# Optimization experiments

Hardware: AMD Instinct MI355X
Metric: run time of the kernel (lower is better)

Reference implementation:

```python
import jax, jax.numpy as jnp
import numpy as np

HID, H, P = 1024, 16, 50  # hid_dim, n_heads, max_relative_position
DH = HID // H


def _rel_idx(len_q, len_k):
    # [Lq, Lk] clipped relative-distance indices into the (2P+1)-row table
    d = jnp.arange(len_k)[None, :] - jnp.arange(len_q)[:, None]
    return jnp.clip(d, -P, P) + P


def setup_inputs() -> dict:
    key = jax.random.key(0)
    ks = jax.random.split(key, 13)
    L, B = 2048, 2
    s = 0.02
    return {
        "query": jax.random.normal(ks[0], (L, B, HID), jnp.float32),
        "key": jax.random.normal(ks[1], (L, B, HID), jnp.float32),
        "value": jax.random.normal(ks[2], (L, B, HID), jnp.float32),
        "Wq": jax.random.normal(ks[3], (HID, HID), jnp.float32) * s,
        "bq": jax.random.normal(ks[4], (HID,), jnp.float32) * s,
        "Wk": jax.random.normal(ks[5], (HID, HID), jnp.float32) * s,
        "bk": jax.random.normal(ks[6], (HID,), jnp.float32) * s,
        "Wv": jax.random.normal(ks[7], (HID, HID), jnp.float32) * s,
        "bv": jax.random.normal(ks[8], (HID,), jnp.float32) * s,
        "Wo": jax.random.normal(ks[9], (HID, HID), jnp.float32) * s,
        "bo": jax.random.normal(ks[10], (HID,), jnp.float32) * s,
        "rel_k": jax.random.normal(ks[11], (2 * P + 1, DH), jnp.float32) * s,
        "rel_v": jax.random.normal(ks[12], (2 * P + 1, DH), jnp.float32) * s,
    }


def reference(query, key, value, Wq, bq, Wk, bk, Wv, bv, Wo, bo, rel_k, rel_v):
    # inputs are seq-first [L, B, hid]; torch code transposes to batch-first
    q = jnp.swapaxes(query, 0, 1)  # [B, Lq, hid]
    k = jnp.swapaxes(key, 0, 1)
    v = jnp.swapaxes(value, 0, 1)
    B, Lq, _ = q.shape
    Lk = k.shape[1]

    q = q @ Wq.T + bq
    k = k @ Wk.T + bk
    v = v @ Wv.T + bv

    # split heads: [B, H, L, DH]
    qh = q.reshape(B, Lq, H, DH).transpose(0, 2, 1, 3)
    kh = k.reshape(B, Lk, H, DH).transpose(0, 2, 1, 3)
    vh = v.reshape(B, Lk, H, DH).transpose(0, 2, 1, 3)

    idx = _rel_idx(Lq, Lk)
    Rk = rel_k[idx]  # [Lq, Lk, DH]
    Rv = rel_v[idx]  # [Lq, Lk, DH]

    attn1 = jnp.einsum('bhqd,bhkd->bhqk', qh, kh)
    attn2 = jnp.einsum('bhqd,qkd->bhqk', qh, Rk)
    scale = jnp.asarray(np.sqrt(DH), qh.dtype)
    attn = jax.nn.softmax((attn1 + attn2) / scale, axis=-1)  # dropout p=0 -> identity

    w1 = jnp.einsum('bhqk,bhkd->bhqd', attn, vh)
    w2 = jnp.einsum('bhqk,qkd->bhqd', attn, Rv)
    x = (w1 + w2).transpose(0, 2, 1, 3).reshape(B, Lq, HID)
    x = x @ Wo.T + bo
    return jnp.swapaxes(x, 0, 1)  # [Lq, B, hid]
```

## Files before the change

kernel.cpp:

```cpp
#include <hip/hip_runtime.h>


#define LSEQ 2048
#define HIDDIM 1024
#define NH 16
#define DHD 64
#define NREL 101
#define PMAX 50
#define SCL 0.18033688011112042f

typedef __attribute__((ext_vector_type(8))) __bf16 bf16x8;
typedef __attribute__((ext_vector_type(4))) float f32x4;

#define MFMA(A, B, C) __builtin_amdgcn_mfma_f32_16x16x32_bf16(A, B, C, 0, 0, 0)

__device__ __forceinline__ unsigned short f2bf(float f) {
  unsigned int u = __builtin_bit_cast(unsigned int, f);
  u += 0x7fffu + ((u >> 16) & 1u);
  return (unsigned short)(u >> 16);
}
__device__ __forceinline__ float bflo(unsigned int u) { return __builtin_bit_cast(float, u << 16); }

__device__ __forceinline__ uint4 pack8(float4 f0, float4 f1) {
  uint4 o;
  o.x = (unsigned)f2bf(f0.x) | ((unsigned)f2bf(f0.y) << 16);
  o.y = (unsigned)f2bf(f0.z) | ((unsigned)f2bf(f0.w) << 16);
  o.z = (unsigned)f2bf(f1.x) | ((unsigned)f2bf(f1.y) << 16);
  o.w = (unsigned)f2bf(f1.z) | ((unsigned)f2bf(f1.w) << 16);
  return o;
}

__device__ __forceinline__ void gload16(const unsigned short* g, unsigned short* l) {
  __builtin_amdgcn_global_load_lds(
      (const __attribute__((address_space(1))) unsigned int*)g,
      (__attribute__((address_space(3))) unsigned int*)l, 16, 0, 0);
}

__global__ void cast_w4(const float* __restrict__ s0, const float* __restrict__ s1,
                        const float* __restrict__ s2, const float* __restrict__ s3,
                        unsigned short* __restrict__ dst) {
  const int e = (blockIdx.x * 256 + threadIdx.x) * 8;
  const int g = e >> 20;
  const float* s = (g == 0) ? s0 : (g == 1) ? s1 : (g == 2) ? s2 : s3;
  const int o = e & 0xFFFFF;
  const float4 f0 = *(const float4*)(s + o);
  const float4 f1 = *(const float4*)(s + o + 4);
  *(uint4*)(dst + e) = pack8(f0, f1);
}

__global__ void cast_x3(const float* __restrict__ q, const float* __restrict__ k,
                        const float* __restrict__ v,
                        unsigned short* __restrict__ dq, unsigned short* __restrict__ dk,
                        unsigned short* __restrict__ dv) {
  const int gid = blockIdx.x * 256 + threadIdx.x;
  const int segi = gid >> 19;
  const int e = (gid & 0x7FFFF) * 8;
  const float* s = (segi == 0) ? q : (segi == 1) ? k : v;
  unsigned short* dst = (segi == 0) ? dq : (segi == 1) ? dk : dv;
  const int m = e >> 10, kk = e & 1023;
  const int b = m >> 11, l = m & 2047;
  const float* sp = s + (size_t)((l << 1) + b) * HIDDIM + kk;
  const float4 f0 = *(const float4*)sp;
  const float4 f1 = *(const float4*)(sp + 4);
  *(uint4*)(dst + e) = pack8(f0, f1);
}

__global__ void cast_rk_kernel(const float* __restrict__ src, unsigned short* __restrict__ dst) {
  const int e = blockIdx.x * 256 + threadIdx.x;
  if (e >= 112 * 64) return;
  dst[e] = (e < NREL * 64) ? f2bf(src[e]) : (unsigned short)0;
}

__global__ void cast_rv_kernel(const float* __restrict__ src, unsigned short* __restrict__ dst) {
  const int e = blockIdx.x * 256 + threadIdx.x;
  if (e >= 64 * 128) return;
  const int d = e >> 7, j = e & 127;
  dst[e] = (j < NREL) ? f2bf(src[j * DHD + d]) : (unsigned short)0;
}

__global__ __launch_bounds__(256, 3) void gemm_qkv(
    const unsigned short* __restrict__ Xq, const unsigned short* __restrict__ Xk,
    const unsigned short* __restrict__ Xv, const unsigned short* __restrict__ Wcat,
    const float* __restrict__ bq, const float* __restrict__ bk, const float* __restrict__ bv,
    unsigned short* __restrict__ Qb, unsigned short* __restrict__ Kb,
    unsigned short* __restrict__ Vgt) {
  __shared__ __align__(16) unsigned short SH[17408];
  unsigned short* LA = SH;
  unsigned short* LB = SH + 8192;

  const int tid = threadIdx.x;
  const int seg = blockIdx.x >> 8;
  const int t = blockIdx.x & 255;
  const int m0 = (t >> 3) * 128, n0 = (t & 7) * 128;

  const unsigned short* A = (seg == 0) ? Xq : (seg == 1) ? Xk : Xv;
  const unsigned short* W = Wcat + ((size_t)seg << 20);
  const float* bias = (seg == 0) ? bq : (seg == 1) ? bk : bv;

  const int lane = tid & 63, w = tid >> 6;
  const int c = lane & 15, quad = lane >> 4;

  const int srow = w * 32 + (lane >> 3);
  const int scol = ((lane & 7) ^ (lane >> 3)) << 3;
  const unsigned short* pA = A + (size_t)(m0 + srow) * 1024 + scol;
  const unsigned short* pW = W + (size_t)(n0 + srow) * 1024 + scol;
  unsigned short* lA = LA + w * 2048;
  unsigned short* lB = LB + w * 2048;

  const int wr = w >> 1, wc = w & 1;
  const int cx = (c & 7) << 3;

  f32x4 acc[4][4] = {};

  for (int k0 = 0; k0 < 1024; k0 += 64) {
#pragma unroll
    for (int i = 0; i < 4; i++) {
      gload16(pA + k0 + i * 8192, lA + i * 512);
      gload16(pW + k0 + i * 8192, lB + i * 512);
    }
    __syncthreads();
#pragma unroll
    for (int ks = 0; ks < 2; ks++) {
      bf16x8 af[4], bfr[4];
#pragma unroll
      for (int f = 0; f < 4; f++) {
        af[f]  = *(const bf16x8*)&LA[(wr * 64 + f * 16 + c) * 64 + ((ks * 32 + quad * 8) ^ cx)];
        bfr[f] = *(const bf16x8*)&LB[(wc * 64 + f * 16 + c) * 64 + ((ks * 32 + quad * 8) ^ cx)];
      }
#pragma unroll
      for (int i = 0; i < 4; i++)
#pragma unroll
        for (int j = 0; j < 4; j++)
          acc[i][j] = MFMA(af[i], bfr[j], acc[i][j]);
    }
    __syncthreads();
  }

  const int b = m0 >> 11, l0 = m0 & 2047;
  const int h0 = n0 >> 6;
  if (seg < 2) {
    unsigned short* out = seg ? Kb : Qb;
#pragma unroll
    for (int i = 0; i < 4; i++)
#pragma unroll
      for (int j = 0; j < 4; j++) {
        const int nl = wc * 64 + j * 16 + c;
        const float bv_ = bias[n0 + nl];
        const int h = h0 + (nl >> 6), d = nl & 63;
#pragma unroll
        for (int r = 0; r < 4; r++) {
          const int l = l0 + wr * 64 + i * 16 + quad * 4 + r;
          out[((size_t)((b * NH + h) * LSEQ + l) << 6) + d] = f2bf(acc[i][j][r] + bv_);
        }
      }
  } else {
    unsigned short* Ct = SH;
#pragma unroll
    for (int i = 0; i < 4; i++)
#pragma unroll
      for (int j = 0; j < 4; j++) {
        const int nl = wc * 64 + j * 16 + c;
        const float bv_ = bias[n0 + nl];
#pragma unroll
        for (int r = 0; r < 4; r++) {
          const int ml = wr * 64 + i * 16 + quad * 4 + r;
          Ct[nl * 136 + ml] = f2bf(acc[i][j][r] + bv_);
        }
      }
    __syncthreads();
    const int dr = tid >> 1, lc = (tid & 1) * 64;
    const int h = h0 + (dr >> 6), dd = dr & 63;
    unsigned short* dst = Vgt + ((size_t)((b * NH + h) * 64 + dd)) * LSEQ + l0 + lc;
    const unsigned short* src = Ct + dr * 136 + lc;
#pragma unroll
    for (int u = 0; u < 8; u++)
      *(uint4*)(dst + u * 8) = *(const uint4*)(src + u * 8);
  }
}

template <int MODE>
__global__ __launch_bounds__(256, 4) void gemm64(
    const unsigned short* __restrict__ A,
    const unsigned short* __restrict__ W,
    const float* __restrict__ bias,
    float* __restrict__ outF,
    unsigned short* __restrict__ outB) {
  constexpr int K = 1024;
  __shared__ unsigned short As[64 * 72];
  __shared__ unsigned short Bs[64 * 72];
  const int tid = threadIdx.x;
  const int tm = blockIdx.x >> 4, tn = blockIdx.x & 15;
  const int m0 = tm * 64, n0 = tn * 64;
  const int lane = tid & 63, wave = tid >> 6;
  const int wm = (wave >> 1) * 32, wn = (wave & 1) * 32;
  const int qr = lane & 15, quad = lane >> 4;
  const int sr = tid >> 3, sc = (tid & 7) * 8;
  f32x4 acc[2][2] = {};
  for (int k0 = 0; k0 < K; k0 += 64) {
    *(uint4*)&As[sr * 72 + sc]        = *(const uint4*)&A[(size_t)(m0 + sr) * K + k0 + sc];
    *(uint4*)&As[(sr + 32) * 72 + sc] = *(const uint4*)&A[(size_t)(m0 + sr + 32) * K + k0 + sc];
    *(uint4*)&Bs[sr * 72 + sc]        = *(const uint4*)&W[(size_t)(n0 + sr) * K + k0 + sc];
    *(uint4*)&Bs[(sr + 32) * 72 + sc] = *(const uint4*)&W[(size_t)(n0 + sr + 32) * K + k0 + sc];
    __syncthreads();
#pragma unroll
    for (int ks = 0; ks < 64; ks += 32) {
      bf16x8 a0 = *(const bf16x8*)&As[(wm + qr) * 72 + ks + quad * 8];
      bf16x8 a1 = *(const bf16x8*)&As[(wm + 16 + qr) * 72 + ks + quad * 8];
      bf16x8 b0 = *(const bf16x8*)&Bs[(wn + qr) * 72 + ks + quad * 8];
      bf16x8 b1 = *(const bf16x8*)&Bs[(wn + 16 + qr) * 72 + ks + quad * 8];
      acc[0][0] = MFMA(a0, b0, acc[0][0]);
      acc[0][1] = MFMA(a0, b1, acc[0][1]);
      acc[1][0] = MFMA(a1, b0, acc[1][0]);
      acc[1][1] = MFMA(a1, b1, acc[1][1]);
    }
    __syncthreads();
  }
#pragma unroll
  for (int i = 0; i < 2; i++)
#pragma unroll
    for (int j = 0; j < 2; j++) {
      const int n = n0 + wn + 16 * j + qr;
      const float bv = bias[n];
#pragma unroll
      for (int rr = 0; rr < 4; rr++) {
        const int m = m0 + wm + 16 * i + quad * 4 + rr;
        const float v = acc[i][j][rr] + bv;
        const int b = m >> 11, l = m & 2047;
        if (MODE == 1) {
          outF[(size_t)((l << 1) + b) * HIDDIM + n] = v;
        }
      }
    }
}

#define KT 32
__global__ __launch_bounds__(256, 4) void attn_mfma(
    const unsigned short* __restrict__ Qb,
    const unsigned short* __restrict__ Kb,
    const unsigned short* __restrict__ Vgt,
    const unsigned short* __restrict__ RKb,
    const unsigned short* __restrict__ RVb,
    unsigned short* __restrict__ outB) {
  __shared__ __align__(16) unsigned short SH[20416];
  unsigned short* Kst = SH;
  unsigned short* Tb  = SH + 7424;
  unsigned short* SrS = SH + 13952;

  const int tid = threadIdx.x;
  const int xcd = blockIdx.x & 7, slot = blockIdx.x >> 3;
  const int bh = (slot >> 5) * 8 + xcd;
  const int q0 = (slot & 31) * 64;

  const int lane = tid & 63, wq = tid >> 6;
  const int c = lane & 15, quad = lane >> 4;
  const size_t base = (size_t)bh * (LSEQ * DHD);
  const unsigned short* Qp = Qb + base;
  const unsigned short* Kp = Kb + base;
  const unsigned short* Vp = Vgt + base;
  unsigned short* Ptw = SH + 4608 + wq * 704;

  const int qrow_w = q0 + wq * 16;
  const int srow = quad * 4;
  const int wrow0 = wq * 16 + srow;

  {
    unsigned* tz = (unsigned*)(Tb + wq * 1632);
    for (int e = lane; e < 816; e += 64) tz[e] = 0u;
  }

  const bf16x8 aq0 = *(const bf16x8*)&Qp[(size_t)(qrow_w + c) * DHD + quad * 8];
  const bf16x8 aq1 = *(const bf16x8*)&Qp[(size_t)(qrow_w + c) * DHD + 32 + quad * 8];

#pragma unroll
  for (int jt = 0; jt < 7; jt++) {
    bf16x8 b0 = *(const bf16x8*)&RKb[(jt * 16 + c) * DHD + quad * 8];
    bf16x8 b1 = *(const bf16x8*)&RKb[(jt * 16 + c) * DHD + 32 + quad * 8];
    f32x4 s4 = {};
    s4 = MFMA(aq0, b0, s4);
    s4 = MFMA(aq1, b1, s4);
    const int jc = jt * 16 + c;
    if (jc < NREL) {
#pragma unroll
      for (int r = 0; r < 4; r++) SrS[(wrow0 + r) * NREL + jc] = f2bf(s4[r]);
    }
  }

  float Srlo[4], Srhi[4];
#pragma unroll
  for (int r = 0; r < 4; r++) {
    Srlo[r] = bflo((unsigned)SrS[(wrow0 + r) * NREL + 0]);
    Srhi[r] = bflo((unsigned)SrS[(wrow0 + r) * NREL + 100]);
  }

  float rsum[4] = {0.f, 0.f, 0.f, 0.f};
  float lows[4] = {0.f, 0.f, 0.f, 0.f}, highs[4] = {0.f, 0.f, 0.f, 0.f};
  f32x4 Od[4] = {};

  const int strow = tid >> 3, stcol = (tid & 7) * 8;

  {
    uint4 k0r = *(const uint4*)&Kp[(size_t)strow * DHD + stcol];
    *(uint4*)&Kst[strow * 72 + stcol] = k0r;
  }
  __syncthreads();

  for (int it = 0; it < 64; ++it) {
    const int k0 = it * KT;
    const int cur = (it & 1) * 2304;
    uint4 kreg;
    if (it < 63) kreg = *(const uint4*)&Kp[(size_t)(k0 + KT + strow) * DHD + stcol];
    bf16x8 vf[4];
#pragma unroll
    for (int t = 0; t < 4; t++)
      vf[t] = *(const bf16x8*)&Vp[(size_t)(t * 16 + c) * LSEQ + k0 + quad * 8];

    const bf16x8 bk00 = *(const bf16x8*)&Kst[cur + c * 72 + quad * 8];
    const bf16x8 bk01 = *(const bf16x8*)&Kst[cur + c * 72 + 32 + quad * 8];
    const bf16x8 bk10 = *(const bf16x8*)&Kst[cur + (16 + c) * 72 + quad * 8];
    const bf16x8 bk11 = *(const bf16x8*)&Kst[cur + (16 + c) * 72 + 32 + quad * 8];
    f32x4 s0 = {}, s1 = {};
    s0 = MFMA(aq0, bk00, s0);
    s0 = MFMA(aq1, bk01, s0);
    s1 = MFMA(aq0, bk10, s1);
    s1 = MFMA(aq1, bk11, s1);

    const int mode = (k0 + KT - 1 <= qrow_w - 50) ? 0 : (k0 >= qrow_w + 65) ? 2 : 1;

#pragma unroll
    for (int kt = 0; kt < 2; kt++) {
      const f32x4 s = kt ? s1 : s0;
      const int kcol = k0 + kt * 16 + c;
#pragma unroll
      for (int r = 0; r < 4; r++) {
        float srv;
        int j = -1;
        if (mode == 0) srv = Srlo[r];
        else if (mode == 2) srv = Srhi[r];
        else {
          int dl = kcol - (qrow_w + srow + r);
          dl = dl < -PMAX ? -PMAX : (dl > PMAX ? PMAX : dl);
          j = dl + PMAX;
          srv = bflo((unsigned)SrS[(wrow0 + r) * NREL + j]);
        }
        const float p = exp2f((s[r] + srv) * SCL);
        const unsigned short pb = f2bf(p);
        const float pf = bflo((unsigned)pb);
        rsum[r] += pf;
        if (mode == 0) lows[r] += pf;
        else if (mode == 2) highs[r] += pf;
        else {
          if (j == 0) lows[r] += pf;
          else if (j == 100) highs[r] += pf;
          else Tb[(wrow0 + r) * 102 + j] = pb;
        }
        Ptw[(srow + r) * 44 + kt * 16 + c] = pb;
      }
    }

    const uint2 aplo = *(const uint2*)&Ptw[c * 44 + quad * 8];
    const uint2 aphi = *(const uint2*)&Ptw[c * 44 + quad * 8 + 4];
    const bf16x8 ap = __builtin_bit_cast(bf16x8, (uint4){aplo.x, aplo.y, aphi.x, aphi.y});
#pragma unroll
    for (int t = 0; t < 4; t++)
      Od[t] = MFMA(ap, vf[t], Od[t]);

    if (it < 63) *(uint4*)&Kst[(cur ^ 2304) + strow * 72 + stcol] = kreg;
    __syncthreads();
  }

#pragma unroll
  for (int m = 1; m < 16; m <<= 1) {
#pragma unroll
    for (int r = 0; r < 4; r++) {
      rsum[r] += __shfl_xor(rsum[r], m, 64);
      lows[r] += __shfl_xor(lows[r], m, 64);
      highs[r] += __shfl_xor(highs[r], m, 64);
    }
  }
  if (c == 0) {
#pragma unroll
    for (int r = 0; r < 4; r++) {
      Tb[(wrow0 + r) * 102 + 0]   = f2bf(lows[r]);
      Tb[(wrow0 + r) * 102 + 100] = f2bf(highs[r]);
    }
  }
  __syncthreads();

#pragma unroll
  for (int kc = 0; kc < 4; kc++) {
    unsigned short a8[8];
#pragma unroll
    for (int jj = 0; jj < 8; jj++) {
      const int j = kc * 32 + quad * 8 + jj;
      a8[jj] = (j <= 100) ? Tb[(wq * 16 + c) * 102 + j] : (unsigned short)0;
    }
    bf16x8 at;
#pragma unroll
    for (int jj = 0; jj < 8; jj++) at[jj] = __builtin_bit_cast(__bf16, a8[jj]);
#pragma unroll
    for (int t = 0; t < 4; t++) {
      const bf16x8 bv = *(const bf16x8*)&RVb[(t * 16 + c) * 128 + kc * 32 + quad * 8];
      Od[t] = MFMA(at, bv, Od[t]);
    }
  }

  const int b = bh >> 4, h = bh & 15;
#pragma unroll
  for (int r = 0; r < 4; r++) {
    const float inv = 1.f / rsum[r];
    const int qg = q0 + wq * 16 + srow + r;
    unsigned short* op = outB + (size_t)(b * LSEQ + qg) * HIDDIM + h * DHD + c;
#pragma unroll
    for (int t = 0; t < 4; t++) op[t * 16] = f2bf(Od[t][r] * inv);
  }
}

extern "C" void kernel_launch(void* const* d_in, const int* in_sizes, int n_in,
                              void* d_out, int out_size, void* d_ws, size_t ws_size,
                              hipStream_t stream) {
  const float* query = (const float*)d_in[0];
  const float* key   = (const float*)d_in[1];
  const float* value = (const float*)d_in[2];
  const float* Wq = (const float*)d_in[3];  const float* bq = (const float*)d_in[4];
  const float* Wk = (const float*)d_in[5];  const float* bk = (const float*)d_in[6];
  const float* Wv = (const float*)d_in[7];  const float* bv = (const float*)d_in[8];
  const float* Wo = (const float*)d_in[9];  const float* bo = (const float*)d_in[10];
  const float* relk = (const float*)d_in[11];
  const float* relv = (const float*)d_in[12];
  float* out = (float*)d_out;

  char* w = (char*)d_ws;
  const size_t MB = 1ull << 20;
  unsigned short* Wcat = (unsigned short*)(w + 0 * MB);
  unsigned short* Wob  = (unsigned short*)(w + 6 * MB);
  unsigned short* Xq   = (unsigned short*)(w + 8 * MB);
  unsigned short* Qb   = (unsigned short*)(w + 16 * MB);
  unsigned short* Kb   = (unsigned short*)(w + 24 * MB);
  unsigned short* Vgt  = (unsigned short*)(w + 32 * MB);
  unsigned short* AOb  = Xq;
  unsigned short* RKb  = Wcat;
  unsigned short* RVb  = (unsigned short*)(w + 2 * MB);
  unsigned short* Xk = (unsigned short*)out;
  unsigned short* Xv = (unsigned short*)out + (4u << 20);

  cast_w4<<<2048, 256, 0, stream>>>(Wq, Wk, Wv, Wo, Wcat);
  cast_x3<<<6144, 256, 0, stream>>>(query, key, value, Xq, Xk, Xv);
  gemm_qkv<<<768, 256, 0, stream>>>(Xq, Xk, Xv, Wcat, bq, bk, bv, Qb, Kb, Vgt);
  cast_rk_kernel<<<28, 256, 0, stream>>>(relk, RKb);
  cast_rv_kernel<<<32, 256, 0, stream>>>(relv, RVb);
  attn_mfma<<<1024, 256, 0, stream>>>(Qb, Kb, Vgt, RKb, RVb, AOb);
  gemm64<1><<<1024, 256, 0, stream>>>(AOb, Wob, bo, out, nullptr);
}
```

Before: 334.8 us.

## Transpose score MFMA so each lane owns a query row, use packed bf16 converts

Swaps the MFMA operand order in the QK and Q·relK products so the score tile is transposed and each lane holds one query row. The softmax row sums then reduce with fewer shuffles, and the relative-bias and Tb tables become per-wave buffers. The change also uses the v_cvt_pk_bf16_f32 instruction for packing and writes P as packed uint2 stores. Block-wide __syncthreads before the rel-V stage are replaced by an LDS waitcnt fence. The aim is to cut scalar bf16 conversion, LDS traffic and shuffle work in the inner softmax loop, at the cost of more intricate per-lane indexing and reliance on per-wave LDS visibility.

```diff
diff --git a/kernel.cpp b/kernel.cpp
--- a/kernel.cpp
+++ b/kernel.cpp
@@ -13,6 +13,7 @@
 typedef __attribute__((ext_vector_type(4))) float f32x4;
 
 #define MFMA(A, B, C) __builtin_amdgcn_mfma_f32_16x16x32_bf16(A, B, C, 0, 0, 0)
+#define LDS_FENCE() asm volatile("s_waitcnt lgkmcnt(0)" ::: "memory")
 
 __device__ __forceinline__ unsigned short f2bf(float f) {
   unsigned int u = __builtin_bit_cast(unsigned int, f);
@@ -20,6 +21,14 @@
   return (unsigned short)(u >> 16);
 }
 __device__ __forceinline__ float bflo(unsigned int u) { return __builtin_bit_cast(float, u << 16); }
+
+__device__ __forceinline__ unsigned cvtpk(float lo, float hi) {
+  unsigned r;
+  asm("v_cvt_pk_bf16_f32 %0, %1, %2" : "=v"(r) : "v"(lo), "v"(hi));
+  return r;
+}
+__device__ __forceinline__ float pklo(unsigned pk) { return __builtin_bit_cast(float, pk << 16); }
+__device__ __forceinline__ float pkhi(unsigned pk) { return __builtin_bit_cast(float, pk & 0xffff0000u); }
 
 __device__ __forceinline__ uint4 pack8(float4 f0, float4 f1) {
   uint4 o;
@@ -241,10 +250,8 @@
     const unsigned short* __restrict__ RKb,
     const unsigned short* __restrict__ RVb,
     unsigned short* __restrict__ outB) {
-  __shared__ __align__(16) unsigned short SH[20416];
+  __shared__ __align__(16) unsigned short SH[20480];
   unsigned short* Kst = SH;
-  unsigned short* Tb  = SH + 7424;
-  unsigned short* SrS = SH + 13952;
 
   const int tid = threadIdx.x;
   const int xcd = blockIdx.x & 7, slot = blockIdx.x >> 3;
@@ -253,19 +260,21 @@
 
   const int lane = tid & 63, wq = tid >> 6;
   const int c = lane & 15, quad = lane >> 4;
+  unsigned short* Ptw = SH + 4608 + wq * 640;
+  unsigned short* Tb  = SH + 7168 + wq * 1664;
+  unsigned short* SrS = SH + 13824 + wq * 1664;
+
   const size_t base = (size_t)bh * (LSEQ * DHD);
   const unsigned short* Qp = Qb + base;
   const unsigned short* Kp = Kb + base;
   const unsigned short* Vp = Vgt + base;
-  unsigned short* Ptw = SH + 4608 + wq * 704;
 
   const int qrow_w = q0 + wq * 16;
-  const int srow = quad * 4;
-  const int wrow0 = wq * 16 + srow;
 
   {
-    unsigned* tz = (unsigned*)(Tb + wq * 1632);
-    for (int e = lane; e < 816; e += 64) tz[e] = 0u;
+    uint4 z = {0u, 0u, 0u, 0u};
+    uint4* tz = (uint4*)(SH + 7168);
+    for (int e = tid; e < 832; e += 256) tz[e] = z;
   }
 
   const bf16x8 aq0 = *(const bf16x8*)&Qp[(size_t)(qrow_w + c) * DHD + quad * 8];
@@ -273,36 +282,30 @@
 
 #pragma unroll
   for (int jt = 0; jt < 7; jt++) {
-    bf16x8 b0 = *(const bf16x8*)&RKb[(jt * 16 + c) * DHD + quad * 8];
-    bf16x8 b1 = *(const bf16x8*)&RKb[(jt * 16 + c) * DHD + 32 + quad * 8];
+    const bf16x8 rk0 = *(const bf16x8*)&RKb[(jt * 16 + c) * DHD + quad * 8];
+    const bf16x8 rk1 = *(const bf16x8*)&RKb[(jt * 16 + c) * DHD + 32 + quad * 8];
     f32x4 s4 = {};
-    s4 = MFMA(aq0, b0, s4);
-    s4 = MFMA(aq1, b1, s4);
-    const int jc = jt * 16 + c;
-    if (jc < NREL) {
-#pragma unroll
-      for (int r = 0; r < 4; r++) SrS[(wrow0 + r) * NREL + jc] = f2bf(s4[r]);
-    }
-  }
-
-  float Srlo[4], Srhi[4];
-#pragma unroll
-  for (int r = 0; r < 4; r++) {
-    Srlo[r] = bflo((unsigned)SrS[(wrow0 + r) * NREL + 0]);
-    Srhi[r] = bflo((unsigned)SrS[(wrow0 + r) * NREL + 100]);
-  }
-
-  float rsum[4] = {0.f, 0.f, 0.f, 0.f};
-  float lows[4] = {0.f, 0.f, 0.f, 0.f}, highs[4] = {0.f, 0.f, 0.f, 0.f};
-  f32x4 Od[4] = {};
+    s4 = MFMA(rk0, aq0, s4);
+    s4 = MFMA(rk1, aq1, s4);
+    const int jb = jt * 16 + quad * 4;
+    const unsigned p01 = cvtpk(s4[0], s4[1]);
+    const unsigned p23 = cvtpk(s4[2], s4[3]);
+    if (jb <= 102)     *(unsigned*)&SrS[c * 104 + jb] = p01;
+    if (jb + 2 <= 102) *(unsigned*)&SrS[c * 104 + jb + 2] = p23;
+  }
 
   const int strow = tid >> 3, stcol = (tid & 7) * 8;
-
   {
     uint4 k0r = *(const uint4*)&Kp[(size_t)strow * DHD + stcol];
     *(uint4*)&Kst[strow * 72 + stcol] = k0r;
   }
   __syncthreads();
+
+  const float srvlo = bflo((unsigned)SrS[c * 104 + 0]);
+  const float srvhi = bflo((unsigned)SrS[c * 104 + 100]);
+
+  float lows = 0.f, highs = 0.f, mids = 0.f;
+  f32x4 Od[4] = {};
 
   for (int it = 0; it < 64; ++it) {
     const int k0 = it * KT;
@@ -314,52 +317,70 @@
     for (int t = 0; t < 4; t++)
       vf[t] = *(const bf16x8*)&Vp[(size_t)(t * 16 + c) * LSEQ + k0 + quad * 8];
 
-    const bf16x8 bk00 = *(const bf16x8*)&Kst[cur + c * 72 + quad * 8];
-    const bf16x8 bk01 = *(const bf16x8*)&Kst[cur + c * 72 + 32 + quad * 8];
-    const bf16x8 bk10 = *(const bf16x8*)&Kst[cur + (16 + c) * 72 + quad * 8];
-    const bf16x8 bk11 = *(const bf16x8*)&Kst[cur + (16 + c) * 72 + 32 + quad * 8];
+    const bf16x8 ka00 = *(const bf16x8*)&Kst[cur + c * 72 + quad * 8];
+    const bf16x8 ka01 = *(const bf16x8*)&Kst[cur + c * 72 + 32 + quad * 8];
+    const bf16x8 ka10 = *(const bf16x8*)&Kst[cur + (16 + c) * 72 + quad * 8];
+    const bf16x8 ka11 = *(const bf16x8*)&Kst[cur + (16 + c) * 72 + 32 + quad * 8];
     f32x4 s0 = {}, s1 = {};
-    s0 = MFMA(aq0, bk00, s0);
-    s0 = MFMA(aq1, bk01, s0);
-    s1 = MFMA(aq0, bk10, s1);
-    s1 = MFMA(aq1, bk11, s1);
+    s0 = MFMA(ka00, aq0, s0);
+    s0 = MFMA(ka01, aq1, s0);
+    s1 = MFMA(ka10, aq0, s1);
+    s1 = MFMA(ka11, aq1, s1);
 
     const int mode = (k0 + KT - 1 <= qrow_w - 50) ? 0 : (k0 >= qrow_w + 65) ? 2 : 1;
 
-#pragma unroll
-    for (int kt = 0; kt < 2; kt++) {
-      const f32x4 s = kt ? s1 : s0;
-      const int kcol = k0 + kt * 16 + c;
+    unsigned pkA0, pkA1, pkB0, pkB1;
+    if (mode != 1) {
+      const float srv = (mode == 0) ? srvlo : srvhi;
+      const float e0 = exp2f((s0[0] + srv) * SCL);
+      const float e1 = exp2f((s0[1] + srv) * SCL);
+      const float e2 = exp2f((s0[2] + srv) * SCL);
+      const float e3 = exp2f((s0[3] + srv) * SCL);
+      const float e4 = exp2f((s1[0] + srv) * SCL);
+      const float e5 = exp2f((s1[1] + srv) * SCL);
+      const float e6 = exp2f((s1[2] + srv) * SCL);
+      const float e7 = exp2f((s1[3] + srv) * SCL);
+      pkA0 = cvtpk(e0, e1); pkA1 = cvtpk(e2, e3);
+      pkB0 = cvtpk(e4, e5); pkB1 = cvtpk(e6, e7);
+      const float sq = ((pklo(pkA0) + pkhi(pkA0)) + (pklo(pkA1) + pkhi(pkA1)))
+                     + ((pklo(pkB0) + pkhi(pkB0)) + (pklo(pkB1) + pkhi(pkB1)));
+      if (mode == 0) lows += sq; else highs += sq;
+    } else {
+      const int kb0 = k0 + quad * 4 - (qrow_w + c) + 50;
+      float ee[8]; int jj[8];
 #pragma unroll
       for (int r = 0; r < 4; r++) {
-        float srv;
-        int j = -1;
-        if (mode == 0) srv = Srlo[r];
-        else if (mode == 2) srv = Srhi[r];
-        else {
-          int dl = kcol - (qrow_w + srow + r);
-          dl = dl < -PMAX ? -PMAX : (dl > PMAX ? PMAX : dl);
-          j = dl + PMAX;
-          srv = bflo((unsigned)SrS[(wrow0 + r) * NREL + j]);
-        }
-        const float p = exp2f((s[r] + srv) * SCL);
-        const unsigned short pb = f2bf(p);
-        const float pf = bflo((unsigned)pb);
-        rsum[r] += pf;
-        if (mode == 0) lows[r] += pf;
-        else if (mode == 2) highs[r] += pf;
-        else {
-          if (j == 0) lows[r] += pf;
-          else if (j == 100) highs[r] += pf;
-          else Tb[(wrow0 + r) * 102 + j] = pb;
-        }
-        Ptw[(srow + r) * 44 + kt * 16 + c] = pb;
-      }
-    }
-
-    const uint2 aplo = *(const uint2*)&Ptw[c * 44 + quad * 8];
-    const uint2 aphi = *(const uint2*)&Ptw[c * 44 + quad * 8 + 4];
-    const bf16x8 ap = __builtin_bit_cast(bf16x8, (uint4){aplo.x, aplo.y, aphi.x, aphi.y});
+        int j0 = kb0 + r;       j0 = j0 < 0 ? 0 : (j0 > 100 ? 100 : j0);
+        int j1 = kb0 + 16 + r;  j1 = j1 < 0 ? 0 : (j1 > 100 ? 100 : j1);
+        jj[r] = j0; jj[4 + r] = j1;
+        const float sv0 = bflo((unsigned)SrS[c * 104 + j0]);
+        const float sv1 = bflo((unsigned)SrS[c * 104 + j1]);
+        ee[r]     = exp2f((s0[r] + sv0) * SCL);
+        ee[4 + r] = exp2f((s1[r] + sv1) * SCL);
+      }
+      pkA0 = cvtpk(ee[0], ee[1]); pkA1 = cvtpk(ee[2], ee[3]);
+      pkB0 = cvtpk(ee[4], ee[5]); pkB1 = cvtpk(ee[6], ee[7]);
+      const unsigned pks[4] = {pkA0, pkA1, pkB0, pkB1};
+#pragma unroll
+      for (int i = 0; i < 4; i++) {
+        const unsigned pk = pks[i];
+        const float plo = pklo(pk), phi = pkhi(pk);
+        const int jl = jj[2 * i], jh = jj[2 * i + 1];
+        if (jl == 0) lows += plo;
+        else if (jl == 100) highs += plo;
+        else { mids += plo; Tb[c * 104 + jl] = (unsigned short)pk; }
+        if (jh == 0) lows += phi;
+        else if (jh == 100) highs += phi;
+        else { mids += phi; Tb[c * 104 + jh] = (unsigned short)(pk >> 16); }
+      }
+    }
+
+    uint2 w0; w0.x = pkA0; w0.y = pkA1;
+    uint2 w1; w1.x = pkB0; w1.y = pkB1;
+    *(uint2*)&Ptw[c * 40 + quad * 4] = w0;
+    *(uint2*)&Ptw[c * 40 + 16 + quad * 4] = w1;
+    LDS_FENCE();
+    const bf16x8 ap = *(const bf16x8*)&Ptw[c * 40 + quad * 8];
 #pragma unroll
     for (int t = 0; t < 4; t++)
       Od[t] = MFMA(ap, vf[t], Od[t]);
@@ -369,34 +390,23 @@
   }
 
 #pragma unroll
-  for (int m = 1; m < 16; m <<= 1) {
-#pragma unroll
-    for (int r = 0; r < 4; r++) {
-      rsum[r] += __shfl_xor(rsum[r], m, 64);
-      lows[r] += __shfl_xor(lows[r], m, 64);
-      highs[r] += __shfl_xor(highs[r], m, 64);
-    }
-  }
-  if (c == 0) {
-#pragma unroll
-    for (int r = 0; r < 4; r++) {
-      Tb[(wrow0 + r) * 102 + 0]   = f2bf(lows[r]);
-      Tb[(wrow0 + r) * 102 + 100] = f2bf(highs[r]);
-    }
-  }
-  __syncthreads();
+  for (int m = 16; m < 64; m <<= 1) {
+    lows  += __shfl_xor(lows,  m, 64);
+    highs += __shfl_xor(highs, m, 64);
+    mids  += __shfl_xor(mids,  m, 64);
+  }
+  const float rsum = (lows + highs) + mids;
+  if (lane < 16) {
+    Tb[c * 104 + 0]   = f2bf(lows);
+    Tb[c * 104 + 100] = f2bf(highs);
+  }
+  LDS_FENCE();
 
 #pragma unroll
   for (int kc = 0; kc < 4; kc++) {
-    unsigned short a8[8];
-#pragma unroll
-    for (int jj = 0; jj < 8; jj++) {
-      const int j = kc * 32 + quad * 8 + jj;
-      a8[jj] = (j <= 100) ? Tb[(wq * 16 + c) * 102 + j] : (unsigned short)0;
-    }
-    bf16x8 at;
-#pragma unroll
-    for (int jj = 0; jj < 8; jj++) at[jj] = __builtin_bit_cast(__bf16, a8[jj]);
+    uint4 zz = {0u, 0u, 0u, 0u};
+    bf16x8 at = __builtin_bit_cast(bf16x8, zz);
+    if (kc < 3 || quad == 0) at = *(const bf16x8*)&Tb[c * 104 + kc * 32 + quad * 8];
 #pragma unroll
     for (int t = 0; t < 4; t++) {
       const bf16x8 bv = *(const bf16x8*)&RVb[(t * 16 + c) * 128 + kc * 32 + quad * 8];
@@ -407,8 +417,9 @@
   const int b = bh >> 4, h = bh & 15;
 #pragma unroll
   for (int r = 0; r < 4; r++) {
-    const float inv = 1.f / rsum[r];
-    const int qg = q0 + wq * 16 + srow + r;
+    const float rs = __shfl(rsum, quad * 4 + r, 64);
+    const float inv = 1.f / rs;
+    const int qg = qrow_w + quad * 4 + r;
     unsigned short* op = outB + (size_t)(b * LSEQ + qg) * HIDDIM + h * DHD + c;
 #pragma unroll
     for (int t = 0; t < 4; t++) op[t * 16] = f2bf(Od[t][r] * inv);
```

Result: no change. 335.8 us (+0.3%).
